# Optimization experiments

Hardware: AMD Instinct MI355X
Metric: run time of the kernel (lower is better)

## Reference

```python
import jax, jax.numpy as jnp
import numpy as np
from jax import lax

B, CIN, COUT, WDIM, K, H, W_ = 8, 512, 512, 512, 3, 64, 64

def setup_inputs() -> dict:
    key = jax.random.key(0)
    ks = jax.random.split(key, 7)
    x = jax.random.normal(ks[0], (B, CIN, H, W_), dtype=jnp.float32)
    w = jax.random.normal(ks[1], (B, WDIM), dtype=jnp.float32)
    noise = jax.random.normal(ks[2], (B, COUT, H, W_), dtype=jnp.float32)
    # params (kaiming-ish scale for weight; demodulation normalizes anyway)
    weight = jax.random.normal(ks[3], (1, COUT, CIN, K, K), dtype=jnp.float32) * 0.05
    affine_w = jax.random.normal(ks[4], (CIN, WDIM), dtype=jnp.float32) * (1.0 / np.sqrt(WDIM))
    affine_b = jnp.zeros((CIN,), dtype=jnp.float32)
    bias = jnp.zeros((COUT,), dtype=jnp.float32)
    return {"x": x, "w": w, "noise": noise, "weight": weight,
            "affine_w": affine_w, "affine_b": affine_b, "bias": bias}

def reference(x, w, noise, weight, affine_w, affine_b, bias):
    b, cin, h, ww = x.shape
    cout, k = weight.shape[1], weight.shape[3]
    # style: affine(w) + 1
    s = jnp.einsum('bd,cd->bc', w, affine_w) + affine_b          # [B, Cin]
    s = s[:, None, :, None, None] + 1.0                           # [B,1,Cin,1,1]
    w_mod = weight * s                                            # [B,Cout,Cin,k,k]
    d = lax.rsqrt(jnp.sum(w_mod * w_mod, axis=(2, 3, 4), keepdims=True) + 1e-8)
    w_mod = w_mod * d
    # grouped conv: groups = B
    x_ = x.reshape(1, b * cin, h, ww)
    w_ = w_mod.reshape(b * cout, cin, k, k)
    pad = k // 2
    y = lax.conv_general_dilated(
        x_, w_, window_strides=(1, 1), padding=[(pad, pad), (pad, pad)],
        feature_group_count=b,
        dimension_numbers=('NCHW', 'OIHW', 'NCHW'))
    y = y.reshape(b, cout, h, ww)
    y = y + noise + bias[None, :, None, None]
    return jnp.where(y >= 0, y, 0.2 * y)
```

## Files before the change

### kernel.cpp

```cpp
#include <hip/hip_runtime.h>
#include <hip/hip_bf16.h>


#define CIN   512
#define COUT  512
#define KDIM  4608
#define HWPIX 4096

typedef __attribute__((ext_vector_type(8))) __bf16 bf16x8;
typedef __attribute__((ext_vector_type(4))) float  f32x4;

__device__ __forceinline__ unsigned short f2bf(float f){
  union { float f; unsigned int u; } v; v.f = f;
  unsigned int u = v.u;
  u += 0x7fffu + ((u >> 16) & 1u);
  return (unsigned short)(u >> 16);
}

#define GLDS16(g, l) __builtin_amdgcn_global_load_lds(                      \
    (const __attribute__((address_space(1))) unsigned int*)(g),             \
    (__attribute__((address_space(3))) unsigned int*)(l), 16, 0, 0)

__global__ void style_k(const float* __restrict__ w, const float* __restrict__ aw,
                        const float* __restrict__ ab, float* __restrict__ styles){
  int wid = threadIdx.x >> 6, lane = threadIdx.x & 63;
  int gid = blockIdx.x * 4 + wid;
  int b = gid >> 9, c = gid & 511;
  const float* wb = w + b * 512;
  const float* ar = aw + c * 512;
  float sum = 0.f;
  for (int j = lane; j < 512; j += 64) sum += wb[j] * ar[j];
  for (int off = 32; off; off >>= 1) sum += __shfl_down(sum, off, 64);
  if (lane == 0) styles[gid] = sum + ab[c] + 1.0f;
}

__global__ void modw_k(const float* __restrict__ weight, const float* __restrict__ styles,
                       unsigned short* __restrict__ wmod){
  int o = blockIdx.x;
  int b = blockIdx.y;
  int t = threadIdx.x;
  const float* wrow = weight + (size_t)o * KDIM;
  const float* st = styles + b * 512;
  __shared__ unsigned short sw[9 * 520];
  __shared__ float red[4];
  int wid = t >> 6, lane = t & 63;
  float vals[18];
  float part = 0.f;
#pragma unroll
  for (int it = 0; it < 9; ++it){
    int e = (it * 256 + t) * 2;
    float2 v2 = *(const float2*)(wrow + e);
    int i0 = e / 9, i1 = (e + 1) / 9;
    float a0 = v2.x * st[i0];
    float a1 = v2.y * st[i1];
    vals[2 * it] = a0; vals[2 * it + 1] = a1;
    part += a0 * a0 + a1 * a1;
  }
  for (int off = 32; off; off >>= 1) part += __shfl_down(part, off, 64);
  if (lane == 0) red[wid] = part;
  __syncthreads();
  float d = rsqrtf(red[0] + red[1] + red[2] + red[3] + 1e-8f);
#pragma unroll
  for (int it = 0; it < 9; ++it){
    int e = (it * 256 + t) * 2;
    int i0 = e / 9, i1 = (e + 1) / 9;
    int tap0 = e - i0 * 9, tap1 = e + 1 - i1 * 9;
    sw[tap0 * 520 + i0] = f2bf(vals[2 * it] * d);
    sw[tap1 * 520 + i1] = f2bf(vals[2 * it + 1] * d);
  }
  __syncthreads();
  unsigned int* orow32 = (unsigned int*)(wmod + ((size_t)(b * 512 + o)) * KDIM);
#pragma unroll
  for (int it = 0; it < 9; ++it){
    int u = it * 256 + t;
    int e = u * 2;
    int tap2 = e >> 9, i2 = e & 511;
    orow32[u] = *(const unsigned int*)&sw[tap2 * 520 + i2];
  }
}

__global__ void xpose_k(const float* __restrict__ x, unsigned short* __restrict__ xpad){
  int h = blockIdx.x, cg = blockIdx.y, b = blockIdx.z;
  int c0 = cg * 64;
  __shared__ unsigned short lds[64][66];
  int t = threadIdx.x;
  const float* xb = x + (((size_t)(b * 512 + c0)) * 64 + h) * 64;
#pragma unroll
  for (int it = 0; it < 4; ++it){
    int idx = it * 256 + t;
    int cl = idx >> 4, w4 = (idx & 15) * 4;
    float4 v = *(const float4*)(xb + (size_t)cl * 4096 + w4);
    lds[w4 + 0][cl] = f2bf(v.x);
    lds[w4 + 1][cl] = f2bf(v.y);
    lds[w4 + 2][cl] = f2bf(v.z);
    lds[w4 + 3][cl] = f2bf(v.w);
  }
  if (t < 64){
    int which = t >> 5;
    int ch2 = (t & 31) * 2;
    int wl = which ? 65 : 0;
    *(unsigned int*)&xpad[(((size_t)b * 66 + h + 1) * 66 + wl) * 512 + c0 + ch2] = 0u;
  }
  if (h == 0 || h == 63){
    int row = (h == 0) ? 0 : 65;
    for (int u = t; u < 66 * 32; u += 256){
      int wl = u >> 5, ch2 = (u & 31) * 2;
      *(unsigned int*)&xpad[(((size_t)b * 66 + row) * 66 + wl) * 512 + c0 + ch2] = 0u;
    }
  }
  __syncthreads();
#pragma unroll
  for (int it = 0; it < 2; ++it){
    int idx = it * 256 + t;
    int wl = idx >> 3, ch = idx & 7;
    unsigned int u0 = *(const unsigned int*)&lds[wl][ch * 8 + 0];
    unsigned int u1 = *(const unsigned int*)&lds[wl][ch * 8 + 2];
    unsigned int u2 = *(const unsigned int*)&lds[wl][ch * 8 + 4];
    unsigned int u3 = *(const unsigned int*)&lds[wl][ch * 8 + 6];
    int off = ((b * 66 + h + 1) * 66 + (wl + 1)) * 512 + c0 + ch * 8;
    *(uint4*)&xpad[off] = make_uint4(u0, u1, u2, u3);
  }
}

__device__ __forceinline__ int bshift_of(int t){
  int tap = t >> 3;
  int dy = (tap * 11) >> 5;
  int dx = tap - dy * 3;
  return (((dy - 1) * 66 + (dx - 1)) << 9) + ((t & 7) << 6);
}

__global__ __launch_bounds__(512, 2) void conv_gemm(
    const unsigned short* __restrict__ wmod, const unsigned short* __restrict__ xpad,
    const float* __restrict__ noise, const float* __restrict__ bias,
    float* __restrict__ out){
  __shared__ unsigned short As[4][128 * 64];
  __shared__ unsigned short Bs[4][128 * 64];
  int g = blockIdx.x;
  int b = g & 7, sl = g >> 3;
  int mt = sl >> 4, nt = sl & 15;
  int m0 = mt * 256, n0 = nt * 256, h0 = nt * 4;
  int tid = threadIdx.x, lane = tid & 63, wid = tid >> 6;
  int wmp = wid >> 2, wnp = wid & 3;
  int lf = lane & 15, lg = lane >> 4;

  const unsigned short* wbase = wmod + ((size_t)(b * 512 + m0)) * KDIM;
  const unsigned short* xb    = xpad + (size_t)b * (66 * 66 * 512);

  int srow  = tid >> 3;
  int sc    = (tid & 7) ^ (srow & 7);
  int aoffg  = srow * KDIM + sc * 8;
  int boffg0 = ((h0 + 1) * 66 + srow + 1) * 512 + sc * 8;
  int boffg1 = ((h0 + 2) * 66 + srow + 1) * 512 + sc * 8;

  int arow[4], brow[2];
#pragma unroll
  for (int i = 0; i < 4; ++i) arow[i] = (wmp * 64 + i * 16 + lf) * 64;
#pragma unroll
  for (int j = 0; j < 2; ++j) brow[j] = (wnp * 32 + j * 16 + lf) * 64;
  int pch0 = ((lg    ) ^ (lane & 7)) * 8;
  int pch1 = ((lg + 4) ^ (lane & 7)) * 8;

  f32x4 acc[2][2][4][2];
#pragma unroll
  for (int a0 = 0; a0 < 2; ++a0)
#pragma unroll
    for (int a1 = 0; a1 < 2; ++a1)
#pragma unroll
      for (int a2 = 0; a2 < 4; ++a2)
#pragma unroll
        for (int a3 = 0; a3 < 2; ++a3) acc[a0][a1][a2][a3] = (f32x4){0.f, 0.f, 0.f, 0.f};

  bf16x8 af0[4][2], af1[4][2], bq0[2][2], bq1[2][2];

#define SBAR0() __builtin_amdgcn_sched_barrier(0)

#define STAGE_A(t_, h_, s_) do {                                              \
    const unsigned short* gpa_ = wbase + (size_t)(h_) * (128 * KDIM) + (t_) * 64; \
    GLDS16(gpa_ + aoffg,             &As[s_][tid * 8]);                       \
    GLDS16(gpa_ + aoffg + 64 * KDIM, &As[s_][(512 + tid) * 8]);               \
  } while (0)

#define STAGE_B(t_, h_, s_) do {                                              \
    const unsigned short* gpb_ = xb + (h_) * (2 * 66 * 512) + bshift_of(t_);  \
    GLDS16(gpb_ + boffg0, &Bs[s_][tid * 8]);                                  \
    GLDS16(gpb_ + boffg1, &Bs[s_][(512 + tid) * 8]);                          \
  } while (0)

#define LOAD_AF1(AF_, s_, fi_) do {                                           \
    AF_[fi_][0] = *(const bf16x8*)&As[s_][arow[fi_] + pch0];                  \
    AF_[fi_][1] = *(const bf16x8*)&As[s_][arow[fi_] + pch1];                  \
  } while (0)

#define LOAD_BQ(B_, s_) do {                                                  \
    _Pragma("unroll") for (int fj_ = 0; fj_ < 2; ++fj_){                      \
      B_[fj_][0] = *(const bf16x8*)&Bs[s_][brow[fj_] + pch0];                 \
      B_[fj_][1] = *(const bf16x8*)&Bs[s_][brow[fj_] + pch1]; }               \
  } while (0)

#define MFMA_Q(MH_, NH_, AF_, B_) do {                                        \
    __builtin_amdgcn_s_setprio(1);                                            \
    _Pragma("unroll") for (int fi_ = 0; fi_ < 4; ++fi_)                       \
    _Pragma("unroll") for (int fj_ = 0; fj_ < 2; ++fj_){                      \
      acc[MH_][NH_][fi_][fj_] = __builtin_amdgcn_mfma_f32_16x16x32_bf16(      \
          AF_[fi_][0], B_[fj_][0], acc[MH_][NH_][fi_][fj_], 0, 0, 0);         \
      acc[MH_][NH_][fi_][fj_] = __builtin_amdgcn_mfma_f32_16x16x32_bf16(      \
          AF_[fi_][1], B_[fj_][1], acc[MH_][NH_][fi_][fj_], 0, 0, 0); }       \
    __builtin_amdgcn_s_setprio(0);                                            \
  } while (0)

#define TAIL6() do { SBAR0();                                                 \
    asm volatile("s_waitcnt lgkmcnt(6)" ::: "memory"); SBAR0(); } while (0)
#define TAIL0() do { SBAR0();                                                 \
    asm volatile("s_waitcnt lgkmcnt(0)" ::: "memory"); SBAR0(); } while (0)
#define PH_END() do { SBAR0(); __builtin_amdgcn_s_barrier(); } while (0)
#define VMW4() asm volatile("s_waitcnt vmcnt(4)" ::: "memory")
#define VMW0() asm volatile("s_waitcnt vmcnt(0)" ::: "memory")

  STAGE_A(0, 0, 0); STAGE_A(0, 1, 1); STAGE_B(0, 0, 0); STAGE_B(0, 1, 1);
  STAGE_A(1, 0, 2); STAGE_B(1, 0, 2); STAGE_B(1, 1, 3); STAGE_A(1, 1, 3);
  VMW0();
  __builtin_amdgcn_s_barrier();
  LOAD_AF1(af0, 0, 0); LOAD_AF1(af0, 0, 1); LOAD_AF1(af0, 0, 2); LOAD_AF1(af0, 0, 3);
  LOAD_BQ(bq0, 0);

#pragma unroll 1
  for (int it = 0; it < 35; ++it){
    int T = it * 2;
    LOAD_BQ(bq1, 1); LOAD_AF1(af1, 1, 0);
    TAIL6(); MFMA_Q(0, 0, af0, bq0); PH_END();
    STAGE_A(T + 2, 0, 0); STAGE_B(T + 2, 0, 0);
    LOAD_AF1(af1, 1, 1); LOAD_AF1(af1, 1, 2); LOAD_AF1(af1, 1, 3);
    TAIL6(); MFMA_Q(0, 1, af0, bq1); PH_END();
    STAGE_B(T + 2, 1, 1);
    LOAD_AF1(af0, 2, 0); LOAD_AF1(af0, 2, 1); LOAD_AF1(af0, 2, 2);
    TAIL6(); MFMA_Q(1, 0, af1, bq0); PH_END();
    STAGE_A(T + 2, 1, 1);
    VMW4();
    LOAD_BQ(bq0, 2); LOAD_AF1(af0, 2, 3);
    TAIL6(); MFMA_Q(1, 1, af1, bq1); PH_END();
    LOAD_BQ(bq1, 3); LOAD_AF1(af1, 3, 0);
    TAIL6(); MFMA_Q(0, 0, af0, bq0); PH_END();
    STAGE_A(T + 3, 0, 2); STAGE_B(T + 3, 0, 2);
    LOAD_AF1(af1, 3, 1); LOAD_AF1(af1, 3, 2); LOAD_AF1(af1, 3, 3);
    TAIL6(); MFMA_Q(0, 1, af0, bq1); PH_END();
    STAGE_B(T + 3, 1, 3);
    LOAD_AF1(af0, 0, 0); LOAD_AF1(af0, 0, 1); LOAD_AF1(af0, 0, 2);
    TAIL6(); MFMA_Q(1, 0, af1, bq0); PH_END();
    STAGE_A(T + 3, 1, 3);
    VMW4();
    LOAD_BQ(bq0, 0); LOAD_AF1(af0, 0, 3);
    TAIL6(); MFMA_Q(1, 1, af1, bq1); PH_END();
  }

  LOAD_BQ(bq1, 1); LOAD_AF1(af1, 1, 0);
  TAIL6(); MFMA_Q(0, 0, af0, bq0); PH_END();
  LOAD_AF1(af1, 1, 1); LOAD_AF1(af1, 1, 2); LOAD_AF1(af1, 1, 3);
  TAIL6(); MFMA_Q(0, 1, af0, bq1); PH_END();
  LOAD_AF1(af0, 2, 0); LOAD_AF1(af0, 2, 1); LOAD_AF1(af0, 2, 2);
  TAIL6(); MFMA_Q(1, 0, af1, bq0); PH_END();
  VMW0();
  LOAD_BQ(bq0, 2); LOAD_AF1(af0, 2, 3);
  TAIL6(); MFMA_Q(1, 1, af1, bq1); PH_END();
  LOAD_BQ(bq1, 3); LOAD_AF1(af1, 3, 0);
  TAIL6(); MFMA_Q(0, 0, af0, bq0); PH_END();
  LOAD_AF1(af1, 3, 1); LOAD_AF1(af1, 3, 2); LOAD_AF1(af1, 3, 3);
  TAIL6(); MFMA_Q(0, 1, af0, bq1); PH_END();
  TAIL0(); MFMA_Q(1, 0, af1, bq0); PH_END();
  TAIL0(); MFMA_Q(1, 1, af1, bq1);

#undef STAGE_A
#undef STAGE_B
#undef LOAD_AF1
#undef LOAD_BQ
#undef MFMA_Q
#undef TAIL6
#undef TAIL0
#undef PH_END
#undef VMW4
#undef VMW0
#undef SBAR0

#pragma unroll
  for (int MH = 0; MH < 2; ++MH)
#pragma unroll
    for (int NH = 0; NH < 2; ++NH)
#pragma unroll
      for (int fi = 0; fi < 4; ++fi)
#pragma unroll
        for (int fj = 0; fj < 2; ++fj){
          int o_base = m0 + MH * 128 + wmp * 64 + fi * 16 + lg * 4;
          int n = n0 + NH * 128 + wnp * 32 + fj * 16 + lf;
#pragma unroll
          for (int r = 0; r < 4; ++r){
            int o = o_base + r;
            size_t idx = ((size_t)(b * 512 + o)) * HWPIX + n;
            float v = acc[MH][NH][fi][fj][r] + noise[idx] + bias[o];
            out[idx] = (v >= 0.f) ? v : 0.2f * v;
          }
        }
}

extern "C" void kernel_launch(void* const* d_in, const int* in_sizes, int n_in,
                              void* d_out, int out_size, void* d_ws, size_t ws_size,
                              hipStream_t stream) {
  const float* x        = (const float*)d_in[0];
  const float* w        = (const float*)d_in[1];
  const float* noise    = (const float*)d_in[2];
  const float* weight   = (const float*)d_in[3];
  const float* affine_w = (const float*)d_in[4];
  const float* affine_b = (const float*)d_in[5];
  const float* bias     = (const float*)d_in[6];
  float* out = (float*)d_out;

  float* styles = (float*)d_ws;
  unsigned short* wmod = (unsigned short*)((char*)d_ws + 16384);
  unsigned short* xpad = (unsigned short*)((char*)d_ws + 16384 + 37748736ull);

  style_k<<<dim3(1024), 256, 0, stream>>>(w, affine_w, affine_b, styles);
  modw_k <<<dim3(512, 8), 256, 0, stream>>>(weight, styles, wmod);
  xpose_k<<<dim3(64, 8, 8), 256, 0, stream>>>(x, xpad);
  conv_gemm<<<dim3(256), 512, 0, stream>>>(wmod, xpad, noise, bias, out);
}
```

Before: 338.0 us.

## Restructure GEMM main loop with double-buffered B fragments and fewer barriers

Reworks the software pipeline of the implicit-GEMM conv main loop. Each stage now loads all A fragments at once and keeps two sets of B fragments, so MFMA quadrants can run on one set while the next set comes in from LDS. Block barriers drop from eight to four per iteration, and the vmcnt waits are relaxed. This aims to cut synchronisation stalls and LDS-latency exposure. In exchange it uses more VGPRs and relies on hand-tuned lgkmcnt counts being correct.

After: 725.8 us. 115% more time.

```diff
diff --git a/kernel.cpp b/kernel.cpp
--- a/kernel.cpp
+++ b/kernel.cpp
@@ -170,7 +170,8 @@
 #pragma unroll
         for (int a3 = 0; a3 < 2; ++a3) acc[a0][a1][a2][a3] = (f32x4){0.f, 0.f, 0.f, 0.f};
 
-  bf16x8 af0[4][2], af1[4][2], bq0[2][2], bq1[2][2];
+  bf16x8 af0[4][2], af1[4][2];
+  bf16x8 bq0a[2][2], bq1a[2][2], bq0b[2][2], bq1b[2][2];
 
 #define SBAR0() __builtin_amdgcn_sched_barrier(0)
 
@@ -186,9 +187,10 @@
     GLDS16(gpb_ + boffg1, &Bs[s_][(512 + tid) * 8]);                          \
   } while (0)
 
-#define LOAD_AF1(AF_, s_, fi_) do {                                           \
-    AF_[fi_][0] = *(const bf16x8*)&As[s_][arow[fi_] + pch0];                  \
-    AF_[fi_][1] = *(const bf16x8*)&As[s_][arow[fi_] + pch1];                  \
+#define LOAD_AF(AF_, s_) do {                                                 \
+    _Pragma("unroll") for (int fi_ = 0; fi_ < 4; ++fi_){                      \
+      AF_[fi_][0] = *(const bf16x8*)&As[s_][arow[fi_] + pch0];                \
+      AF_[fi_][1] = *(const bf16x8*)&As[s_][arow[fi_] + pch1]; }              \
   } while (0)
 
 #define LOAD_BQ(B_, s_) do {                                                  \
@@ -208,75 +210,73 @@
     __builtin_amdgcn_s_setprio(0);                                            \
   } while (0)
 
-#define TAIL6() do { SBAR0();                                                 \
-    asm volatile("s_waitcnt lgkmcnt(6)" ::: "memory"); SBAR0(); } while (0)
-#define TAIL0() do { SBAR0();                                                 \
-    asm volatile("s_waitcnt lgkmcnt(0)" ::: "memory"); SBAR0(); } while (0)
-#define PH_END() do { SBAR0(); __builtin_amdgcn_s_barrier(); } while (0)
-#define VMW4() asm volatile("s_waitcnt vmcnt(4)" ::: "memory")
-#define VMW0() asm volatile("s_waitcnt vmcnt(0)" ::: "memory")
-
-  STAGE_A(0, 0, 0); STAGE_A(0, 1, 1); STAGE_B(0, 0, 0); STAGE_B(0, 1, 1);
+#define LG(n_)  do { asm volatile("s_waitcnt lgkmcnt(" #n_ ")" ::: "memory"); \
+                     SBAR0(); } while (0)
+#define BAR()   do { SBAR0(); __builtin_amdgcn_s_barrier(); SBAR0(); } while (0)
+#define VMW8()  do { asm volatile("s_waitcnt vmcnt(8)" ::: "memory"); } while (0)
+#define VMW0()  do { asm volatile("s_waitcnt vmcnt(0)" ::: "memory"); } while (0)
+
+  STAGE_A(0, 0, 0); STAGE_B(0, 0, 0); STAGE_B(0, 1, 1); STAGE_A(0, 1, 1);
   STAGE_A(1, 0, 2); STAGE_B(1, 0, 2); STAGE_B(1, 1, 3); STAGE_A(1, 1, 3);
   VMW0();
   __builtin_amdgcn_s_barrier();
-  LOAD_AF1(af0, 0, 0); LOAD_AF1(af0, 0, 1); LOAD_AF1(af0, 0, 2); LOAD_AF1(af0, 0, 3);
-  LOAD_BQ(bq0, 0);
+  LOAD_AF(af0, 0); LOAD_BQ(bq0a, 0); LOAD_BQ(bq1a, 1); LOAD_AF(af1, 1);
+  SBAR0();
 
 #pragma unroll 1
   for (int it = 0; it < 35; ++it){
     int T = it * 2;
-    LOAD_BQ(bq1, 1); LOAD_AF1(af1, 1, 0);
-    TAIL6(); MFMA_Q(0, 0, af0, bq0); PH_END();
+    LG(12); MFMA_Q(0, 0, af0, bq0a);
+    LG(8);  MFMA_Q(0, 1, af0, bq1a);
+    LG(0);
+    BAR();
     STAGE_A(T + 2, 0, 0); STAGE_B(T + 2, 0, 0);
-    LOAD_AF1(af1, 1, 1); LOAD_AF1(af1, 1, 2); LOAD_AF1(af1, 1, 3);
-    TAIL6(); MFMA_Q(0, 1, af0, bq1); PH_END();
-    STAGE_B(T + 2, 1, 1);
-    LOAD_AF1(af0, 2, 0); LOAD_AF1(af0, 2, 1); LOAD_AF1(af0, 2, 2);
-    TAIL6(); MFMA_Q(1, 0, af1, bq0); PH_END();
-    STAGE_A(T + 2, 1, 1);
-    VMW4();
-    LOAD_BQ(bq0, 2); LOAD_AF1(af0, 2, 3);
-    TAIL6(); MFMA_Q(1, 1, af1, bq1); PH_END();
-    LOAD_BQ(bq1, 3); LOAD_AF1(af1, 3, 0);
-    TAIL6(); MFMA_Q(0, 0, af0, bq0); PH_END();
+    STAGE_B(T + 2, 1, 1); STAGE_A(T + 2, 1, 1);
+    SBAR0(); VMW8();
+    BAR();
+    LOAD_AF(af0, 2); LOAD_BQ(bq0b, 2); LOAD_BQ(bq1b, 3);
+    SBAR0();
+    MFMA_Q(1, 0, af1, bq0a); MFMA_Q(1, 1, af1, bq1a);
+    LOAD_AF(af1, 3);
+    SBAR0();
+    LG(12); MFMA_Q(0, 0, af0, bq0b);
+    LG(8);  MFMA_Q(0, 1, af0, bq1b);
+    LG(0);
+    BAR();
     STAGE_A(T + 3, 0, 2); STAGE_B(T + 3, 0, 2);
-    LOAD_AF1(af1, 3, 1); LOAD_AF1(af1, 3, 2); LOAD_AF1(af1, 3, 3);
-    TAIL6(); MFMA_Q(0, 1, af0, bq1); PH_END();
-    STAGE_B(T + 3, 1, 3);
-    LOAD_AF1(af0, 0, 0); LOAD_AF1(af0, 0, 1); LOAD_AF1(af0, 0, 2);
-    TAIL6(); MFMA_Q(1, 0, af1, bq0); PH_END();
-    STAGE_A(T + 3, 1, 3);
-    VMW4();
-    LOAD_BQ(bq0, 0); LOAD_AF1(af0, 0, 3);
-    TAIL6(); MFMA_Q(1, 1, af1, bq1); PH_END();
-  }
-
-  LOAD_BQ(bq1, 1); LOAD_AF1(af1, 1, 0);
-  TAIL6(); MFMA_Q(0, 0, af0, bq0); PH_END();
-  LOAD_AF1(af1, 1, 1); LOAD_AF1(af1, 1, 2); LOAD_AF1(af1, 1, 3);
-  TAIL6(); MFMA_Q(0, 1, af0, bq1); PH_END();
-  LOAD_AF1(af0, 2, 0); LOAD_AF1(af0, 2, 1); LOAD_AF1(af0, 2, 2);
-  TAIL6(); MFMA_Q(1, 0, af1, bq0); PH_END();
-  VMW0();
-  LOAD_BQ(bq0, 2); LOAD_AF1(af0, 2, 3);
-  TAIL6(); MFMA_Q(1, 1, af1, bq1); PH_END();
-  LOAD_BQ(bq1, 3); LOAD_AF1(af1, 3, 0);
-  TAIL6(); MFMA_Q(0, 0, af0, bq0); PH_END();
-  LOAD_AF1(af1, 3, 1); LOAD_AF1(af1, 3, 2); LOAD_AF1(af1, 3, 3);
-  TAIL6(); MFMA_Q(0, 1, af0, bq1); PH_END();
-  TAIL0(); MFMA_Q(1, 0, af1, bq0); PH_END();
-  TAIL0(); MFMA_Q(1, 1, af1, bq1);
+    STAGE_B(T + 3, 1, 3); STAGE_A(T + 3, 1, 3);
+    SBAR0(); VMW8();
+    BAR();
+    LOAD_AF(af0, 0); LOAD_BQ(bq0a, 0); LOAD_BQ(bq1a, 1);
+    SBAR0();
+    MFMA_Q(1, 0, af1, bq0b); MFMA_Q(1, 1, af1, bq1b);
+    LOAD_AF(af1, 1);
+    SBAR0();
+  }
+
+  LG(12); MFMA_Q(0, 0, af0, bq0a);
+  LG(8);  MFMA_Q(0, 1, af0, bq1a);
+  LG(0);
+  SBAR0(); VMW0();
+  BAR();
+  LOAD_AF(af0, 2); LOAD_BQ(bq0b, 2); LOAD_BQ(bq1b, 3);
+  SBAR0();
+  MFMA_Q(1, 0, af1, bq0a); MFMA_Q(1, 1, af1, bq1a);
+  LOAD_AF(af1, 3);
+  SBAR0();
+  LG(12); MFMA_Q(0, 0, af0, bq0b);
+  LG(8);  MFMA_Q(0, 1, af0, bq1b);
+  LG(0);
+  MFMA_Q(1, 0, af1, bq0b); MFMA_Q(1, 1, af1, bq1b);
 
 #undef STAGE_A
 #undef STAGE_B
-#undef LOAD_AF1
+#undef LOAD_AF
 #undef LOAD_BQ
 #undef MFMA_Q
-#undef TAIL6
-#undef TAIL0
-#undef PH_END
-#undef VMW4
+#undef LG
+#undef BAR
+#undef VMW8
 #undef VMW0
 #undef SBAR0
 
```
